# Kernel optimization log

Measured on AMD Instinct MI355X. Metric: run time of the kernel, lower is better.

The kernel has to match this reference:

```python
import jax, jax.numpy as jnp
import numpy as np

N, DIM = 4096, 1024

def setup_inputs() -> dict:
    key = jax.random.key(0)
    ks = jax.random.split(key, 5)
    scale = 1.0 / np.sqrt(DIM)
    return {
        "x": jax.random.normal(ks[0], (N, DIM), dtype=jnp.float32),
        "Wq": jax.random.normal(ks[1], (DIM, DIM), dtype=jnp.float32) * scale,
        "bq": jax.random.normal(ks[2], (DIM,), dtype=jnp.float32) * 0.01,
        "Wk": jax.random.normal(ks[3], (DIM, DIM), dtype=jnp.float32) * scale,
        "bk": jax.random.normal(ks[4], (DIM,), dtype=jnp.float32) * 0.01,
    }

def reference(x, Wq, bq, Wk, bk):
    # torch nn.Linear: y = x @ W.T + b
    q = x @ Wq.T + bq            # [N, D]
    k = x @ Wk.T + bk            # [N, D]
    scores = q @ k.T             # [N, N] (no 1/sqrt(d) scaling, as in source)
    attn = jax.nn.softmax(scores, axis=-1)
    return attn @ x              # weighted pooling over raw x (no value proj)
```

## Files before the change

### kernel.cpp

```cpp
#include <hip/hip_runtime.h>
#include <hip/hip_bf16.h>
#include <hip/hip_fp16.h>
#include <stdint.h>


using half8   = __attribute__((ext_vector_type(8))) _Float16;
using float4v = __attribute__((ext_vector_type(4))) float;
using int4v   = __attribute__((ext_vector_type(4))) int;

#define QS        (6.0f / 32768.0f)
#define INV_S     (32768.0f / 6.0f)
#define INV_S256  (128.0f / 6.0f)
#define C_HH      (65536.0f * QS * QS)
#define C_X       (256.0f * QS * QS)

#define SX        (6.0f / 32768.0f)
#define SW        (0.25f / 32768.0f)
#define P_HH      (65536.0f * SX * SW)
#define P_X       (256.0f * SX * SW)

#define GLOAD_LDS16(gptr, ldsptr)                                              \
  __builtin_amdgcn_global_load_lds(                                            \
      (__attribute__((address_space(1))) void*)(uintptr_t)(gptr),              \
      (__attribute__((address_space(3))) void*)(unsigned)(uintptr_t)(ldsptr),  \
      16, 0, 0)

__device__ __forceinline__ void barrier_raw() {
  asm volatile("" ::: "memory");
  __builtin_amdgcn_s_barrier();
  asm volatile("" ::: "memory");
}

__global__ __launch_bounds__(256, 2) void gemm_s_stats(
    const int8_t* __restrict__ Ahi, const int8_t* __restrict__ Alo,
    const int8_t* __restrict__ Bhi, const int8_t* __restrict__ Blo,
    _Float16* __restrict__ E, float2* __restrict__ stats)
{
  __shared__ __align__(16) int8_t sAh[2][128 * 64];
  __shared__ __align__(16) int8_t sAl[2][128 * 64];
  __shared__ __align__(16) int8_t sBh[2][128 * 64];
  __shared__ __align__(16) int8_t sBl[2][128 * 64];

  const int tid  = threadIdx.x;
  const int wave = tid >> 6;
  const int lane = tid & 63;
  const int quad = lane >> 4;
  const int t16  = lane & 15;
  const int wm   = wave & 1;
  const int wn   = wave >> 1;
  const int row0 = blockIdx.y * 128;
  const int col0 = blockIdx.x * 128;

  const int seg  = lane & 3;
  const int rsub = lane >> 2;

  const int offA0 = (row0 + wave * 16 + rsub) * 2048 + seg * 16;
  const int offA1 = offA0 + 64 * 2048;
  const int offB0 = (col0 + wave * 16 + rsub) * 2048 + seg * 16;
  const int offB1 = offB0 + 64 * 2048;
  const int ldsT0 = (wave * 16) * 64;
  const int ldsT1 = (64 + wave * 16) * 64;

  int4v hh[4][4], cc[4][4];
#pragma unroll
  for (int i = 0; i < 4; ++i)
#pragma unroll
    for (int j = 0; j < 4; ++j) {
      hh[i][j] = (int4v){0, 0, 0, 0};
      cc[i][j] = (int4v){0, 0, 0, 0};
    }

  auto stage_k = [&](int ks, int b) {
    const int k0 = ks * 64;
    GLOAD_LDS16(Ahi + offA0 + k0, &sAh[b][ldsT0]);
    GLOAD_LDS16(Ahi + offA1 + k0, &sAh[b][ldsT1]);
    GLOAD_LDS16(Alo + offA0 + k0, &sAl[b][ldsT0]);
    GLOAD_LDS16(Alo + offA1 + k0, &sAl[b][ldsT1]);
    GLOAD_LDS16(Bhi + offB0 + k0, &sBh[b][ldsT0]);
    GLOAD_LDS16(Bhi + offB1 + k0, &sBh[b][ldsT1]);
    GLOAD_LDS16(Blo + offB0 + k0, &sBl[b][ldsT0]);
    GLOAD_LDS16(Blo + offB1 + k0, &sBl[b][ldsT1]);
  };

  stage_k(0, 0);
  asm volatile("s_waitcnt vmcnt(0)" ::: "memory");
  barrier_raw();

  int buf = 0;
  for (int ks = 0; ks < 16; ++ks) {
    if (ks < 15) stage_k(ks + 1, buf ^ 1);

    int4v ah[4], al[4], bh[4], bl[4];
#pragma unroll
    for (int i = 0; i < 4; ++i) {
      const int ao = (wm * 64 + i * 16 + t16) * 64 + quad * 16;
      ah[i] = *(const int4v*)&sAh[buf][ao];
      al[i] = *(const int4v*)&sAl[buf][ao];
    }
#pragma unroll
    for (int j = 0; j < 4; ++j) {
      const int bo = (wn * 64 + j * 16 + t16) * 64 + quad * 16;
      bh[j] = *(const int4v*)&sBh[buf][bo];
      bl[j] = *(const int4v*)&sBl[buf][bo];
    }

    __builtin_amdgcn_s_setprio(1);
#pragma unroll
    for (int i = 0; i < 4; ++i)
#pragma unroll
      for (int j = 0; j < 4; ++j) {
        hh[i][j] = __builtin_amdgcn_mfma_i32_16x16x64_i8(ah[i], bh[j], hh[i][j], 0, 0, 0);
        cc[i][j] = __builtin_amdgcn_mfma_i32_16x16x64_i8(ah[i], bl[j], cc[i][j], 0, 0, 0);
        cc[i][j] = __builtin_amdgcn_mfma_i32_16x16x64_i8(al[i], bh[j], cc[i][j], 0, 0, 0);
      }
    __builtin_amdgcn_s_setprio(0);

    if (ks < 15) asm volatile("s_waitcnt vmcnt(0)" ::: "memory");
    barrier_raw();
    buf ^= 1;
  }

  float* red = (float*)sAh;

  float vv[4][4][4];
  float rmax[4][4];
#pragma unroll
  for (int i = 0; i < 4; ++i)
#pragma unroll
    for (int r = 0; r < 4; ++r) {
      float mx = -3.0e38f;
#pragma unroll
      for (int j = 0; j < 4; ++j) {
        float v = C_HH * (float)hh[i][j][r] + C_X * (float)cc[i][j][r];
        vv[i][j][r] = v;
        mx = fmaxf(mx, v);
      }
      mx = fmaxf(mx, __shfl_xor(mx, 1));
      mx = fmaxf(mx, __shfl_xor(mx, 2));
      mx = fmaxf(mx, __shfl_xor(mx, 4));
      mx = fmaxf(mx, __shfl_xor(mx, 8));
      rmax[i][r] = mx;
    }
  if (t16 == 0) {
#pragma unroll
    for (int i = 0; i < 4; ++i)
#pragma unroll
      for (int r = 0; r < 4; ++r)
        red[wn * 128 + wm * 64 + i * 16 + quad * 4 + r] = rmax[i][r];
  }
  __syncthreads();

  float mrow[4][4];
#pragma unroll
  for (int i = 0; i < 4; ++i)
#pragma unroll
    for (int r = 0; r < 4; ++r) {
      const int row = wm * 64 + i * 16 + quad * 4 + r;
      mrow[i][r] = fmaxf(red[row], red[128 + row]);
    }

  float rsum[4][4];
#pragma unroll
  for (int i = 0; i < 4; ++i)
#pragma unroll
    for (int r = 0; r < 4; ++r) {
      float s = 0.f;
#pragma unroll
      for (int j = 0; j < 4; ++j) {
        float e = __expf(vv[i][j][r] - mrow[i][r]);
        vv[i][j][r] = e;
        s += e;
      }
      s += __shfl_xor(s, 1);
      s += __shfl_xor(s, 2);
      s += __shfl_xor(s, 4);
      s += __shfl_xor(s, 8);
      rsum[i][r] = s;
    }
  if (t16 == 0) {
#pragma unroll
    for (int i = 0; i < 4; ++i)
#pragma unroll
      for (int r = 0; r < 4; ++r)
        red[256 + wn * 128 + wm * 64 + i * 16 + quad * 4 + r] = rsum[i][r];
  }
  __syncthreads();

#pragma unroll
  for (int i = 0; i < 4; ++i) {
#pragma unroll
    for (int j = 0; j < 4; ++j) {
#pragma unroll
      for (int r = 0; r < 4; ++r) {
        const int crow = row0 + wm * 64 + i * 16 + quad * 4 + r;
        const int ccol = col0 + wn * 64 + j * 16 + t16;
        E[(size_t)crow * 4096 + ccol] = (_Float16)vv[i][j][r];
      }
    }
  }
  if (wn == 0 && t16 == 0) {
#pragma unroll
    for (int i = 0; i < 4; ++i)
#pragma unroll
      for (int r = 0; r < 4; ++r) {
        const int row = wm * 64 + i * 16 + quad * 4 + r;
        const float l = red[256 + row] + red[256 + 128 + row];
        stats[(size_t)(row0 + row) * 32 + blockIdx.x] =
            make_float2(mrow[i][r], l);
      }
  }
}

__global__ __launch_bounds__(256, 2) void gemm_proj_i8(
    const int8_t* __restrict__ Ahi, const int8_t* __restrict__ Alo,
    const int8_t* __restrict__ Bhi, const int8_t* __restrict__ Blo,
    const float* __restrict__ biasQ, const float* __restrict__ biasK,
    int8_t* __restrict__ Ch, int8_t* __restrict__ Cl)
{
  __shared__ __align__(16) int8_t sAh[2][128 * 64];
  __shared__ __align__(16) int8_t sAl[2][128 * 64];
  __shared__ __align__(16) int8_t sBh[2][128 * 64];
  __shared__ __align__(16) int8_t sBl[2][128 * 64];

  const int tid  = threadIdx.x;
  const int wave = tid >> 6;
  const int lane = tid & 63;
  const int quad = lane >> 4;
  const int t16  = lane & 15;
  const int wm   = wave & 1;
  const int wn   = wave >> 1;
  const int row0 = blockIdx.y * 128;
  const int col0 = blockIdx.x * 128;

  const int seg  = lane & 3;
  const int rsub = lane >> 2;

  const int offA0 = (row0 + wave * 16 + rsub) * 1024 + seg * 16;
  const int offA1 = offA0 + 64 * 1024;
  const int offB0 = (col0 + wave * 16 + rsub) * 1024 + seg * 16;
  const int offB1 = offB0 + 64 * 1024;
  const int ldsT0 = (wave * 16) * 64;
  const int ldsT1 = (64 + wave * 16) * 64;

  int4v hh[4][4], cc[4][4];
#pragma unroll
  for (int i = 0; i < 4; ++i)
#pragma unroll
    for (int j = 0; j < 4; ++j) {
      hh[i][j] = (int4v){0, 0, 0, 0};
      cc[i][j] = (int4v){0, 0, 0, 0};
    }

  auto stage_k = [&](int ks, int b) {
    const int k0 = ks * 64;
    GLOAD_LDS16(Ahi + offA0 + k0, &sAh[b][ldsT0]);
    GLOAD_LDS16(Ahi + offA1 + k0, &sAh[b][ldsT1]);
    GLOAD_LDS16(Alo + offA0 + k0, &sAl[b][ldsT0]);
    GLOAD_LDS16(Alo + offA1 + k0, &sAl[b][ldsT1]);
    GLOAD_LDS16(Bhi + offB0 + k0, &sBh[b][ldsT0]);
    GLOAD_LDS16(Bhi + offB1 + k0, &sBh[b][ldsT1]);
    GLOAD_LDS16(Blo + offB0 + k0, &sBl[b][ldsT0]);
    GLOAD_LDS16(Blo + offB1 + k0, &sBl[b][ldsT1]);
  };

  stage_k(0, 0);
  asm volatile("s_waitcnt vmcnt(0)" ::: "memory");
  barrier_raw();

  int buf = 0;
  for (int ks = 0; ks < 16; ++ks) {
    if (ks < 15) stage_k(ks + 1, buf ^ 1);

    int4v ah[4], al[4], bh[4], bl[4];
#pragma unroll
    for (int i = 0; i < 4; ++i) {
      const int ao = (wm * 64 + i * 16 + t16) * 64 + quad * 16;
      ah[i] = *(const int4v*)&sAh[buf][ao];
      al[i] = *(const int4v*)&sAl[buf][ao];
    }
#pragma unroll
    for (int j = 0; j < 4; ++j) {
      const int bo = (wn * 64 + j * 16 + t16) * 64 + quad * 16;
      bh[j] = *(const int4v*)&sBh[buf][bo];
      bl[j] = *(const int4v*)&sBl[buf][bo];
    }

    __builtin_amdgcn_s_setprio(1);
#pragma unroll
    for (int i = 0; i < 4; ++i)
#pragma unroll
      for (int j = 0; j < 4; ++j) {
        hh[i][j] = __builtin_amdgcn_mfma_i32_16x16x64_i8(ah[i], bh[j], hh[i][j], 0, 0, 0);
        cc[i][j] = __builtin_amdgcn_mfma_i32_16x16x64_i8(ah[i], bl[j], cc[i][j], 0, 0, 0);
        cc[i][j] = __builtin_amdgcn_mfma_i32_16x16x64_i8(al[i], bh[j], cc[i][j], 0, 0, 0);
      }
    __builtin_amdgcn_s_setprio(0);

    if (ks < 15) asm volatile("s_waitcnt vmcnt(0)" ::: "memory");
    barrier_raw();
    buf ^= 1;
  }

#pragma unroll
  for (int i = 0; i < 4; ++i) {
#pragma unroll
    for (int j = 0; j < 4; ++j) {
      const int ccol = col0 + wn * 64 + j * 16 + t16;
      const float* bp = (ccol < 1024) ? biasQ : (biasK - 1024);
#pragma unroll
      for (int r = 0; r < 4; ++r) {
        const int crow = row0 + wm * 64 + i * 16 + quad * 4 + r;
        float v = P_HH * (float)hh[i][j][r] + P_X * (float)cc[i][j][r] + bp[ccol];
        int hi = (int)lrintf(v * INV_S256);
        hi = hi > 127 ? 127 : (hi < -127 ? -127 : hi);
        int lo = (int)lrintf(v * INV_S - 256.0f * (float)hi);
        lo = lo > 127 ? 127 : (lo < -127 ? -127 : lo);
        Ch[(size_t)crow * 2048 + ccol] = (int8_t)hi;
        Cl[(size_t)crow * 2048 + ccol] = (int8_t)lo;
      }
    }
  }
}

__global__ __launch_bounds__(512) void gemm_av(
    const uint16_t* __restrict__ E, const uint16_t* __restrict__ B,
    const float2* __restrict__ stats, float* __restrict__ out)
{
  __shared__ __align__(16) uint16_t stg[2][2][16384];
  __shared__ float betaS[128 * 33];

  const int L      = blockIdx.x;
  const int xcd    = L & 7;
  const int rest   = L >> 3;
  const int colb   = rest & 7;
  const int bandHi = rest >> 3;
  const int band   = xcd + 8 * bandHi;
  const int row0   = band * 128;
  const int col0   = colb * 128;

  const int tid  = threadIdx.x;
  const int wave = tid >> 6;
  const int z    = wave >> 2;
  const int gw   = wave & 3;
  const int lane = tid & 63;
  const int quad = lane >> 4;
  const int t16  = lane & 15;
  const int wm   = gw & 1;
  const int wn   = gw >> 1;

  const int c8   = lane & 7;
  const int r8   = lane >> 3;
  const int srcC = (c8 - r8) & 7;

  int offA[4], offB[4];
#pragma unroll
  for (int r = 0; r < 4; ++r) {
    offA[r] = (row0 + r * 32 + gw * 8 + r8) * 4096 + srcC * 8;
    offB[r] = (col0 + r * 32 + gw * 8 + r8) * 4096 + srcC * 8;
  }

  auto stage_s = [&](int s, int b) {
    const int k0h = (z * 16 + (s >> 1)) * 128 + (s & 1) * 64;
    uint16_t* sA = &stg[b][z][0];
    uint16_t* sB = &stg[b][z][8192];
#pragma unroll
    for (int r = 0; r < 4; ++r) {
      GLOAD_LDS16(E + offA[r] + k0h, &sA[(r * 32 + gw * 8) * 64]);
      GLOAD_LDS16(B + offB[r] + k0h, &sB[(r * 32 + gw * 8) * 64]);
    }
  };

  stage_s(0, 0);

  if (tid < 128) {
    const int row = row0 + tid;
    float2 st[32];
    float m = -3.0e38f;
#pragma unroll
    for (int t = 0; t < 32; ++t) {
      st[t] = stats[(size_t)row * 32 + t];
      m = fmaxf(m, st[t].x);
    }
    float l = 0.f;
#pragma unroll
    for (int t = 0; t < 32; ++t) l += st[t].y * __expf(st[t].x - m);
    const float inv = 1.0f / l;
#pragma unroll
    for (int t = 0; t < 32; ++t)
      betaS[tid * 33 + t] = __expf(st[t].x - m) * inv;
  }
  asm volatile("s_waitcnt vmcnt(0)" ::: "memory");
  __syncthreads();

  float4v acc[4][4];
#pragma unroll
  for (int i = 0; i < 4; ++i)
#pragma unroll
    for (int j = 0; j < 4; ++j)
      acc[i][j] = (float4v){0.f, 0.f, 0.f, 0.f};

  int buf = 0;
  for (int s = 0; s < 32; ++s) {
    if (s < 31) stage_s(s + 1, buf ^ 1);

    const int t = z * 16 + (s >> 1);
    _Float16 bb[4];
#pragma unroll
    for (int i = 0; i < 4; ++i)
      bb[i] = (_Float16)betaS[(wm * 64 + i * 16 + t16) * 33 + t];

    const uint16_t* sA = &stg[buf][z][0];
    const uint16_t* sB = &stg[buf][z][8192];

    half8 af[2][4], bf[2][4];
#pragma unroll
    for (int ks = 0; ks < 2; ++ks) {
#pragma unroll
      for (int i = 0; i < 4; ++i) {
        const int row = wm * 64 + i * 16 + t16;
        const int ch  = (ks * 4 + quad + (t16 & 7)) & 7;
        af[ks][i] = *(const half8*)&sA[row * 64 + ch * 8];
        half8 bs;
#pragma unroll
        for (int c = 0; c < 8; ++c) bs[c] = bb[i];
        af[ks][i] = af[ks][i] * bs;
      }
#pragma unroll
      for (int j = 0; j < 4; ++j) {
        const int row = wn * 64 + j * 16 + t16;
        const int ch  = (ks * 4 + quad + (t16 & 7)) & 7;
        bf[ks][j] = *(const half8*)&sB[row * 64 + ch * 8];
      }
    }

    __builtin_amdgcn_s_setprio(1);
#pragma unroll
    for (int ks = 0; ks < 2; ++ks)
#pragma unroll
      for (int i = 0; i < 4; ++i)
#pragma unroll
        for (int j = 0; j < 4; ++j)
          acc[i][j] = __builtin_amdgcn_mfma_f32_16x16x32_f16(af[ks][i], bf[ks][j], acc[i][j], 0, 0, 0);
    __builtin_amdgcn_s_setprio(0);

    if (s < 31) asm volatile("s_waitcnt vmcnt(0)" ::: "memory");
    barrier_raw();
    buf ^= 1;
  }

  float* xfer = (float*)stg;
#pragma unroll
  for (int h = 0; h < 2; ++h) {
    if (z == 1) {
#pragma unroll
      for (int i = 2 * h; i < 2 * h + 2; ++i)
#pragma unroll
        for (int j = 0; j < 4; ++j)
#pragma unroll
          for (int r = 0; r < 4; ++r) {
            const int e = (i - 2 * h) * 16 + j * 4 + r;
            xfer[e * 256 + gw * 64 + lane] = acc[i][j][r];
          }
    }
    __syncthreads();
    if (z == 0) {
#pragma unroll
      for (int i = 2 * h; i < 2 * h + 2; ++i)
#pragma unroll
        for (int j = 0; j < 4; ++j)
#pragma unroll
          for (int r = 0; r < 4; ++r) {
            const int e = (i - 2 * h) * 16 + j * 4 + r;
            acc[i][j][r] += xfer[e * 256 + gw * 64 + lane];
          }
    }
    __syncthreads();
  }

  if (z == 0) {
#pragma unroll
    for (int i = 0; i < 4; ++i) {
#pragma unroll
      for (int j = 0; j < 4; ++j) {
        const int ccol = col0 + wn * 64 + j * 16 + t16;
#pragma unroll
        for (int r = 0; r < 4; ++r) {
          const int crow = row0 + wm * 64 + i * 16 + quad * 4 + r;
          out[(size_t)crow * 1024 + ccol] = acc[i][j][r];
        }
      }
    }
  }
}

__global__ __launch_bounds__(256) void quantT(
    const float* __restrict__ x, const float* __restrict__ Wq,
    const float* __restrict__ Wk,
    int8_t* __restrict__ xhi, int8_t* __restrict__ xlo,
    int8_t* __restrict__ whi, int8_t* __restrict__ wlo,
    uint16_t* __restrict__ xT)
{
  if (blockIdx.x < 6144) {
    int i = blockIdx.x * 256 + threadIdx.x;
    const float* src; int8_t* dh; int8_t* dl; int idx; float s256, s;
    if (i < 1048576)      { src = x;  idx = i;           dh = xhi; dl = xlo;
                            s256 = INV_S256; s = INV_S; }
    else if (i < 1310720) { src = Wq; idx = i - 1048576; dh = whi; dl = wlo;
                            s256 = 512.0f; s = 131072.0f; }
    else                  { src = Wk; idx = i - 1310720; dh = whi + 1048576;
                            dl = wlo + 1048576; s256 = 512.0f; s = 131072.0f; }
    float4 v = ((const float4*)src)[idx];
    float vv[4] = {v.x, v.y, v.z, v.w};
    int hp = 0, lp = 0;
#pragma unroll
    for (int c = 0; c < 4; ++c) {
      int h = (int)lrintf(vv[c] * s256);
      h = h > 127 ? 127 : (h < -127 ? -127 : h);
      int l = (int)lrintf(vv[c] * s - 256.0f * (float)h);
      l = l > 127 ? 127 : (l < -127 ? -127 : l);
      hp |= (h & 0xff) << (8 * c);
      lp |= (l & 0xff) << (8 * c);
    }
    ((int*)dh)[idx] = hp;
    ((int*)dl)[idx] = lp;
  } else {
    __shared__ float tile[32][33];
    const int tb = blockIdx.x - 6144;
    const int bx = tb & 31;
    const int by = tb >> 5;
    const int tx = threadIdx.x & 31;
    const int ty = threadIdx.x >> 5;
#pragma unroll
    for (int p = 0; p < 4; ++p) {
      const int row = by * 32 + ty + p * 8;
      tile[ty + p * 8][tx] = x[(size_t)row * 1024 + bx * 32 + tx];
    }
    __syncthreads();
#pragma unroll
    for (int p = 0; p < 4; ++p) {
      const int oc = ty + p * 8;
      __half hv = __float2half_rn(tile[tx][oc]);
      xT[(size_t)(bx * 32 + oc) * 4096 + by * 32 + tx] = *(uint16_t*)&hv;
    }
  }
}

extern "C" void kernel_launch(void* const* d_in, const int* in_sizes, int n_in,
                              void* d_out, int out_size, void* d_ws, size_t ws_size,
                              hipStream_t stream) {
  const int N = 4096, D = 1024;
  const float* x  = (const float*)d_in[0];
  const float* Wq = (const float*)d_in[1];
  const float* bq = (const float*)d_in[2];
  const float* Wk = (const float*)d_in[3];
  const float* bk = (const float*)d_in[4];
  float* out = (float*)d_out;

  char* w = (char*)d_ws;
  const size_t MiB = 1024 * 1024;
  int8_t*    xq_hi  = (int8_t*)   (w + 0  * MiB);
  int8_t*    xq_lo  = (int8_t*)   (w + 4  * MiB);
  int8_t*    Wqk_hi = (int8_t*)   (w + 8  * MiB);
  int8_t*    Wqk_lo = (int8_t*)   (w + 10 * MiB);
  int8_t*    qk_hi  = (int8_t*)   (w + 12 * MiB);
  int8_t*    qk_lo  = (int8_t*)   (w + 20 * MiB);
  _Float16*  E      = (_Float16*) (w + 36 * MiB);
  float2*    stats  = (float2*)   (w + 68 * MiB);
  uint16_t*  xTh    = (uint16_t*) (w + 72 * MiB);

  quantT<<<10240, 256, 0, stream>>>(x, Wq, Wk, xq_hi, xq_lo, Wqk_hi, Wqk_lo,
                                    xTh);

  gemm_proj_i8<<<dim3(2048 / 128, N / 128), 256, 0, stream>>>(
      xq_hi, xq_lo, Wqk_hi, Wqk_lo, bq, bk, qk_hi, qk_lo);

  gemm_s_stats<<<dim3(N / 128, N / 128), 256, 0, stream>>>(
      qk_hi, qk_lo, qk_hi + 1024, qk_lo + 1024, E, stats);

  gemm_av<<<256, 512, 0, stream>>>((const uint16_t*)E, xTh, stats, out);

  (void)in_sizes; (void)n_in; (void)out_size; (void)ws_size;
}
```

Before: 218.9 us.

## Stage GEMM epilogues through swizzled LDS for coalesced vector global stores

The three GEMM kernels now write their output tiles into a swizzled shared-memory image, then read them back row-wise and store 16-byte vectors to global memory. Previously each lane issued scalar 2-byte, 1-byte or 4-byte stores scattered across rows. For the projection kernel the hi/lo int8 pair is packed into 16-bit LDS entries and unpacked into separate 8-byte stores. This adds an LDS round trip and an extra barrier per tile in exchange for far fewer, fully coalesced global store transactions.

```diff
diff --git a/kernel.cpp b/kernel.cpp
--- a/kernel.cpp
+++ b/kernel.cpp
@@ -7,6 +7,7 @@
 using half8   = __attribute__((ext_vector_type(8))) _Float16;
 using float4v = __attribute__((ext_vector_type(4))) float;
 using int4v   = __attribute__((ext_vector_type(4))) int;
+using uint2v  = __attribute__((ext_vector_type(2))) unsigned int;
 
 #define QS        (6.0f / 32768.0f)
 #define INV_S     (32768.0f / 6.0f)
@@ -31,15 +32,20 @@
   asm volatile("" ::: "memory");
 }
 
+__device__ __forceinline__ int swz3(int row) {
+  return (((row >> 2) & 3) << 1) ^ (row & 3);
+}
+
 __global__ __launch_bounds__(256, 2) void gemm_s_stats(
     const int8_t* __restrict__ Ahi, const int8_t* __restrict__ Alo,
     const int8_t* __restrict__ Bhi, const int8_t* __restrict__ Blo,
     _Float16* __restrict__ E, float2* __restrict__ stats)
 {
-  __shared__ __align__(16) int8_t sAh[2][128 * 64];
-  __shared__ __align__(16) int8_t sAl[2][128 * 64];
-  __shared__ __align__(16) int8_t sBh[2][128 * 64];
-  __shared__ __align__(16) int8_t sBl[2][128 * 64];
+  __shared__ __align__(16) int8_t smem[65536];
+  int8_t* sAh = smem;
+  int8_t* sAl = smem + 16384;
+  int8_t* sBh = smem + 32768;
+  int8_t* sBl = smem + 49152;
 
   const int tid  = threadIdx.x;
   const int wave = tid >> 6;
@@ -72,14 +78,14 @@
 
   auto stage_k = [&](int ks, int b) {
     const int k0 = ks * 64;
-    GLOAD_LDS16(Ahi + offA0 + k0, &sAh[b][ldsT0]);
-    GLOAD_LDS16(Ahi + offA1 + k0, &sAh[b][ldsT1]);
-    GLOAD_LDS16(Alo + offA0 + k0, &sAl[b][ldsT0]);
-    GLOAD_LDS16(Alo + offA1 + k0, &sAl[b][ldsT1]);
-    GLOAD_LDS16(Bhi + offB0 + k0, &sBh[b][ldsT0]);
-    GLOAD_LDS16(Bhi + offB1 + k0, &sBh[b][ldsT1]);
-    GLOAD_LDS16(Blo + offB0 + k0, &sBl[b][ldsT0]);
-    GLOAD_LDS16(Blo + offB1 + k0, &sBl[b][ldsT1]);
+    GLOAD_LDS16(Ahi + offA0 + k0, sAh + b * 8192 + ldsT0);
+    GLOAD_LDS16(Ahi + offA1 + k0, sAh + b * 8192 + ldsT1);
+    GLOAD_LDS16(Alo + offA0 + k0, sAl + b * 8192 + ldsT0);
+    GLOAD_LDS16(Alo + offA1 + k0, sAl + b * 8192 + ldsT1);
+    GLOAD_LDS16(Bhi + offB0 + k0, sBh + b * 8192 + ldsT0);
+    GLOAD_LDS16(Bhi + offB1 + k0, sBh + b * 8192 + ldsT1);
+    GLOAD_LDS16(Blo + offB0 + k0, sBl + b * 8192 + ldsT0);
+    GLOAD_LDS16(Blo + offB1 + k0, sBl + b * 8192 + ldsT1);
   };
 
   stage_k(0, 0);
@@ -93,15 +99,15 @@
     int4v ah[4], al[4], bh[4], bl[4];
 #pragma unroll
     for (int i = 0; i < 4; ++i) {
-      const int ao = (wm * 64 + i * 16 + t16) * 64 + quad * 16;
-      ah[i] = *(const int4v*)&sAh[buf][ao];
-      al[i] = *(const int4v*)&sAl[buf][ao];
+      const int ao = buf * 8192 + (wm * 64 + i * 16 + t16) * 64 + quad * 16;
+      ah[i] = *(const int4v*)(sAh + ao);
+      al[i] = *(const int4v*)(sAl + ao);
     }
 #pragma unroll
     for (int j = 0; j < 4; ++j) {
-      const int bo = (wn * 64 + j * 16 + t16) * 64 + quad * 16;
-      bh[j] = *(const int4v*)&sBh[buf][bo];
-      bl[j] = *(const int4v*)&sBl[buf][bo];
+      const int bo = buf * 8192 + (wn * 64 + j * 16 + t16) * 64 + quad * 16;
+      bh[j] = *(const int4v*)(sBh + bo);
+      bl[j] = *(const int4v*)(sBl + bo);
     }
 
     __builtin_amdgcn_s_setprio(1);
@@ -120,7 +126,7 @@
     buf ^= 1;
   }
 
-  float* red = (float*)sAh;
+  float* red = (float*)smem;
 
   float vv[4][4][4];
   float rmax[4][4];
@@ -184,20 +190,30 @@
       for (int r = 0; r < 4; ++r)
         red[256 + wn * 128 + wm * 64 + i * 16 + quad * 4 + r] = rsum[i][r];
   }
+
+  uint16_t* img = (uint16_t*)(smem + 32768);
+#pragma unroll
+  for (int i = 0; i < 4; ++i)
+#pragma unroll
+    for (int j = 0; j < 4; ++j)
+#pragma unroll
+      for (int r = 0; r < 4; ++r) {
+        const int row  = wm * 64 + i * 16 + quad * 4 + r;
+        const int col  = wn * 64 + j * 16 + t16;
+        const int colS = col ^ (((quad << 1) ^ r) << 3);
+        _Float16 h = (_Float16)vv[i][j][r];
+        img[row * 128 + colS] = *(const uint16_t*)&h;
+      }
   __syncthreads();
 
 #pragma unroll
-  for (int i = 0; i < 4; ++i) {
-#pragma unroll
-    for (int j = 0; j < 4; ++j) {
-#pragma unroll
-      for (int r = 0; r < 4; ++r) {
-        const int crow = row0 + wm * 64 + i * 16 + quad * 4 + r;
-        const int ccol = col0 + wn * 64 + j * 16 + t16;
-        E[(size_t)crow * 4096 + ccol] = (_Float16)vv[i][j][r];
-      }
-    }
-  }
+  for (int it = 0; it < 8; ++it) {
+    const int row    = wave * 32 + it * 4 + quad;
+    const int chunkS = t16 ^ swz3(row);
+    int4v v = *(const int4v*)&img[row * 128 + chunkS * 8];
+    *(int4v*)&E[(size_t)(row0 + row) * 4096 + col0 + t16 * 8] = v;
+  }
+
   if (wn == 0 && t16 == 0) {
 #pragma unroll
     for (int i = 0; i < 4; ++i)
@@ -217,10 +233,11 @@
     const float* __restrict__ biasQ, const float* __restrict__ biasK,
     int8_t* __restrict__ Ch, int8_t* __restrict__ Cl)
 {
-  __shared__ __align__(16) int8_t sAh[2][128 * 64];
-  __shared__ __align__(16) int8_t sAl[2][128 * 64];
-  __shared__ __align__(16) int8_t sBh[2][128 * 64];
-  __shared__ __align__(16) int8_t sBl[2][128 * 64];
+  __shared__ __align__(16) int8_t smem[65536];
+  int8_t* sAh = smem;
+  int8_t* sAl = smem + 16384;
+  int8_t* sBh = smem + 32768;
+  int8_t* sBl = smem + 49152;
 
   const int tid  = threadIdx.x;
   const int wave = tid >> 6;
@@ -253,14 +270,14 @@
 
   auto stage_k = [&](int ks, int b) {
     const int k0 = ks * 64;
-    GLOAD_LDS16(Ahi + offA0 + k0, &sAh[b][ldsT0]);
-    GLOAD_LDS16(Ahi + offA1 + k0, &sAh[b][ldsT1]);
-    GLOAD_LDS16(Alo + offA0 + k0, &sAl[b][ldsT0]);
-    GLOAD_LDS16(Alo + offA1 + k0, &sAl[b][ldsT1]);
-    GLOAD_LDS16(Bhi + offB0 + k0, &sBh[b][ldsT0]);
-    GLOAD_LDS16(Bhi + offB1 + k0, &sBh[b][ldsT1]);
-    GLOAD_LDS16(Blo + offB0 + k0, &sBl[b][ldsT0]);
-    GLOAD_LDS16(Blo + offB1 + k0, &sBl[b][ldsT1]);
+    GLOAD_LDS16(Ahi + offA0 + k0, sAh + b * 8192 + ldsT0);
+    GLOAD_LDS16(Ahi + offA1 + k0, sAh + b * 8192 + ldsT1);
+    GLOAD_LDS16(Alo + offA0 + k0, sAl + b * 8192 + ldsT0);
+    GLOAD_LDS16(Alo + offA1 + k0, sAl + b * 8192 + ldsT1);
+    GLOAD_LDS16(Bhi + offB0 + k0, sBh + b * 8192 + ldsT0);
+    GLOAD_LDS16(Bhi + offB1 + k0, sBh + b * 8192 + ldsT1);
+    GLOAD_LDS16(Blo + offB0 + k0, sBl + b * 8192 + ldsT0);
+    GLOAD_LDS16(Blo + offB1 + k0, sBl + b * 8192 + ldsT1);
   };
 
   stage_k(0, 0);
@@ -274,15 +291,15 @@
     int4v ah[4], al[4], bh[4], bl[4];
 #pragma unroll
     for (int i = 0; i < 4; ++i) {
-      const int ao = (wm * 64 + i * 16 + t16) * 64 + quad * 16;
-      ah[i] = *(const int4v*)&sAh[buf][ao];
-      al[i] = *(const int4v*)&sAl[buf][ao];
+      const int ao = buf * 8192 + (wm * 64 + i * 16 + t16) * 64 + quad * 16;
+      ah[i] = *(const int4v*)(sAh + ao);
+      al[i] = *(const int4v*)(sAl + ao);
     }
 #pragma unroll
     for (int j = 0; j < 4; ++j) {
-      const int bo = (wn * 64 + j * 16 + t16) * 64 + quad * 16;
-      bh[j] = *(const int4v*)&sBh[buf][bo];
-      bl[j] = *(const int4v*)&sBl[buf][bo];
+      const int bo = buf * 8192 + (wn * 64 + j * 16 + t16) * 64 + quad * 16;
+      bh[j] = *(const int4v*)(sBh + bo);
+      bl[j] = *(const int4v*)(sBl + bo);
     }
 
     __builtin_amdgcn_s_setprio(1);
@@ -301,6 +318,7 @@
     buf ^= 1;
   }
 
+  uint16_t* img = (uint16_t*)(smem + 32768);
 #pragma unroll
   for (int i = 0; i < 4; ++i) {
 #pragma unroll
@@ -309,16 +327,39 @@
       const float* bp = (ccol < 1024) ? biasQ : (biasK - 1024);
 #pragma unroll
       for (int r = 0; r < 4; ++r) {
-        const int crow = row0 + wm * 64 + i * 16 + quad * 4 + r;
         float v = P_HH * (float)hh[i][j][r] + P_X * (float)cc[i][j][r] + bp[ccol];
         int hi = (int)lrintf(v * INV_S256);
         hi = hi > 127 ? 127 : (hi < -127 ? -127 : hi);
         int lo = (int)lrintf(v * INV_S - 256.0f * (float)hi);
         lo = lo > 127 ? 127 : (lo < -127 ? -127 : lo);
-        Ch[(size_t)crow * 2048 + ccol] = (int8_t)hi;
-        Cl[(size_t)crow * 2048 + ccol] = (int8_t)lo;
-      }
-    }
+        const int row  = wm * 64 + i * 16 + quad * 4 + r;
+        const int col  = wn * 64 + j * 16 + t16;
+        const int colS = col ^ (((quad << 1) ^ r) << 3);
+        img[row * 128 + colS] = (uint16_t)((hi & 0xff) | ((lo & 0xff) << 8));
+      }
+    }
+  }
+  __syncthreads();
+
+#pragma unroll
+  for (int it = 0; it < 8; ++it) {
+    const int row    = wave * 32 + it * 4 + quad;
+    const int chunkS = t16 ^ swz3(row);
+    int4v p = *(const int4v*)&img[row * 128 + chunkS * 8];
+    const unsigned w0 = (unsigned)p[0], w1 = (unsigned)p[1];
+    const unsigned w2 = (unsigned)p[2], w3 = (unsigned)p[3];
+    uint2v hw, lw;
+    hw[0] = (w0 & 0xffu) | (((w0 >> 16) & 0xffu) << 8) |
+            ((w1 & 0xffu) << 16) | (((w1 >> 16) & 0xffu) << 24);
+    hw[1] = (w2 & 0xffu) | (((w2 >> 16) & 0xffu) << 8) |
+            ((w3 & 0xffu) << 16) | (((w3 >> 16) & 0xffu) << 24);
+    lw[0] = ((w0 >> 8) & 0xffu) | (((w0 >> 24) & 0xffu) << 8) |
+            (((w1 >> 8) & 0xffu) << 16) | ((w1 >> 24) << 24);
+    lw[1] = ((w2 >> 8) & 0xffu) | (((w2 >> 24) & 0xffu) << 8) |
+            (((w3 >> 8) & 0xffu) << 16) | ((w3 >> 24) << 24);
+    const size_t go = (size_t)(row0 + row) * 2048 + col0 + t16 * 8;
+    *(uint2v*)&Ch[go] = hw;
+    *(uint2v*)&Cl[go] = lw;
   }
 }
 
@@ -477,19 +518,29 @@
     __syncthreads();
   }
 
+  float* img = (float*)((int8_t*)stg + 65536);
   if (z == 0) {
 #pragma unroll
-    for (int i = 0; i < 4; ++i) {
-#pragma unroll
-      for (int j = 0; j < 4; ++j) {
-        const int ccol = col0 + wn * 64 + j * 16 + t16;
+    for (int i = 0; i < 4; ++i)
+#pragma unroll
+      for (int j = 0; j < 4; ++j)
 #pragma unroll
         for (int r = 0; r < 4; ++r) {
-          const int crow = row0 + wm * 64 + i * 16 + quad * 4 + r;
-          out[(size_t)crow * 1024 + ccol] = acc[i][j][r];
+          const int row  = wm * 64 + i * 16 + quad * 4 + r;
+          const int col  = wn * 64 + j * 16 + t16;
+          const int colS = col ^ (((quad << 1) ^ r) << 2);
+          img[row * 128 + colS] = acc[i][j][r];
         }
-      }
-    }
+  }
+  __syncthreads();
+
+#pragma unroll
+  for (int it = 0; it < 8; ++it) {
+    const int row    = wave * 16 + (lane >> 2);
+    const int chunk  = (lane & 3) * 8 + it;
+    const int chunkS = chunk ^ swz3(row);
+    float4v v = *(const float4v*)&img[row * 128 + chunkS * 4];
+    *(float4v*)&out[(size_t)(row0 + row) * 1024 + col0 + chunk * 4] = v;
   }
 }
 
```

Result: no change. 218.2 us (-0.3%).
